# Kernel optimization log

Measured on AMD Instinct MI355X. Metric: run time of the kernel, lower is better.

## Reference

```python
import jax, jax.numpy as jnp
import numpy as np

NUM_ATOMS = 40000
NUM_EDGES = 640000
FAN_IN = 128
NFM = 128
FAN_OUT = 128


def setup_inputs() -> dict:
    key = jax.random.key(0)
    k1, k2, k3, k4, k5, k6, k7 = jax.random.split(key, 7)
    x = jax.random.normal(k1, (NUM_ATOMS, FAN_IN), dtype=jnp.float32)
    w_ij = jax.random.normal(k2, (NUM_EDGES, NFM), dtype=jnp.float32)
    seg_i = jnp.sort(jax.random.randint(k3, (NUM_EDGES,), 0, NUM_ATOMS))
    idx_j = jax.random.randint(k4, (NUM_EDGES,), 0, NUM_ATOMS)
    # learned params: in2fac (no bias), fac2out (bias)
    W_in = jax.random.normal(k5, (FAN_IN, NFM), dtype=jnp.float32) / np.sqrt(FAN_IN)
    W_out = jax.random.normal(k6, (NFM, FAN_OUT), dtype=jnp.float32) / np.sqrt(NFM)
    b_out = jax.random.normal(k7, (FAN_OUT,), dtype=jnp.float32) * 0.01
    return {"x": x, "w_ij": w_ij, "seg_i": seg_i, "idx_j": idx_j,
            "seg_i_sum": NUM_ATOMS, "W_in": W_in, "W_out": W_out, "b_out": b_out}


def reference(x, w_ij, seg_i, idx_j, seg_i_sum, W_in, W_out, b_out):
    # in2fac: Dense without bias  (num_atoms, nFM)
    f = x @ W_in
    # gather features of atom j per interaction  (num_edges, nFM)
    f_j = jnp.take(f, idx_j, axis=0)
    # elementwise filter multiply
    wf = w_ij * f_j
    # segment-sum pool over interactions of each atom i  (num_atoms, nFM)
    conv = jax.ops.segment_sum(wf, seg_i, num_segments=seg_i_sum)
    # fac2out: Dense with bias, activation=None
    return conv @ W_out + b_out
```

## Files before the change

kernel.cpp:

```cpp
#include <hip/hip_runtime.h>

#define NUM_ATOMS 40000
#define NUM_EDGES 640000

__global__ void k_rowstart(const int* __restrict__ seg, int* __restrict__ rs) {
  const int i = blockIdx.x * blockDim.x + threadIdx.x;
  if (i > NUM_ATOMS) return;
  int lo = 0, hi = NUM_EDGES;
  while (lo < hi) {
    const int mid = (lo + hi) >> 1;
    if (seg[mid] < i) lo = mid + 1; else hi = mid;
  }
  rs[i] = lo;
}

__global__ __launch_bounds__(512, 2) void k_gemm1(
    const float* __restrict__ x, const float* __restrict__ Win,
    float* __restrict__ f) {
  __shared__ float xT[128 * 128];
  __shared__ float Wl[128 * 128];
  const int t = threadIdx.x;
  const int m0 = blockIdx.x * 128;

  {
    const float4* Wg = (const float4*)Win;
    float4* Ws = (float4*)Wl;
#pragma unroll
    for (int i = 0; i < 8; ++i) Ws[t + i * 512] = Wg[t + i * 512];
  }
  {
    const int m = t & 127;
    const int kq = t >> 7;
    int mg = m0 + m;
    if (mg >= NUM_ATOMS) mg = NUM_ATOMS - 1;
    const float4* xg = (const float4*)(x + (size_t)mg * 128);
#pragma unroll
    for (int i = 0; i < 8; ++i) {
      const int k4 = kq + i * 4;
      const float4 v = xg[k4];
      const int k = k4 * 4;
      xT[(k + 0) * 128 + m] = v.x;
      xT[(k + 1) * 128 + m] = v.y;
      xT[(k + 2) * 128 + m] = v.z;
      xT[(k + 3) * 128 + m] = v.w;
    }
  }
  __syncthreads();

  const int tx = t & 31;
  const int ty = t >> 5;
  float acc[8][4];
#pragma unroll
  for (int i = 0; i < 8; ++i)
#pragma unroll
    for (int j = 0; j < 4; ++j) acc[i][j] = 0.f;

#pragma unroll 4
  for (int k = 0; k < 128; ++k) {
    const float4 a0 = *(const float4*)&xT[k * 128 + 4 * ty];
    const float4 a1 = *(const float4*)&xT[k * 128 + 64 + 4 * ty];
    const float2 b0 = *(const float2*)&Wl[k * 128 + 2 * tx];
    const float2 b1 = *(const float2*)&Wl[k * 128 + 64 + 2 * tx];
    const float av[8] = {a0.x, a0.y, a0.z, a0.w, a1.x, a1.y, a1.z, a1.w};
    const float bv[4] = {b0.x, b0.y, b1.x, b1.y};
#pragma unroll
    for (int i = 0; i < 8; ++i)
#pragma unroll
      for (int j = 0; j < 4; ++j) acc[i][j] += av[i] * bv[j];
  }

#pragma unroll
  for (int i = 0; i < 8; ++i) {
    const int m = (i < 4) ? (4 * ty + i) : (64 + 4 * ty + (i - 4));
    const int mg = m0 + m;
    if (mg < NUM_ATOMS) {
      float2* o = (float2*)(f + (size_t)mg * 128);
      o[tx]      = make_float2(acc[i][0], acc[i][1]);
      o[32 + tx] = make_float2(acc[i][2], acc[i][3]);
    }
  }
}

__global__ __launch_bounds__(256, 2) void k_conv_out(
    const float* __restrict__ f, const float* __restrict__ w_ij,
    const int* __restrict__ idx_j, const int* __restrict__ rs,
    const float* __restrict__ Wout, const float* __restrict__ bout,
    float* __restrict__ out) {
  __shared__ float Wl[128 * 128];
  __shared__ float conv[32 * 128];
  const int t = threadIdx.x;

  {
    const float4* Wg = (const float4*)Wout;
    float4* Ws = (float4*)Wl;
#pragma unroll
    for (int i = 0; i < 16; ++i) Ws[t + i * 256] = Wg[t + i * 256];
  }

  const int wv = t >> 6;
  const int l = t & 63;
  const int abase = blockIdx.x * 32;

#pragma unroll 1
  for (int ai = 0; ai < 8; ++ai) {
    const int al = wv * 8 + ai;
    const int a = abase + al;
    float accx = 0.f, accy = 0.f;
    const int e0 = rs[a];
    const int e1 = rs[a + 1];
    int e = e0;
    for (; e + 4 <= e1; e += 4) {
      const int j0 = idx_j[e + 0];
      const int j1 = idx_j[e + 1];
      const int j2 = idx_j[e + 2];
      const int j3 = idx_j[e + 3];
      const float2 w0 = ((const float2*)(w_ij + (size_t)(e + 0) * 128))[l];
      const float2 w1 = ((const float2*)(w_ij + (size_t)(e + 1) * 128))[l];
      const float2 w2 = ((const float2*)(w_ij + (size_t)(e + 2) * 128))[l];
      const float2 w3 = ((const float2*)(w_ij + (size_t)(e + 3) * 128))[l];
      const float2 f0 = ((const float2*)(f + (size_t)j0 * 128))[l];
      const float2 f1 = ((const float2*)(f + (size_t)j1 * 128))[l];
      const float2 f2 = ((const float2*)(f + (size_t)j2 * 128))[l];
      const float2 f3 = ((const float2*)(f + (size_t)j3 * 128))[l];
      accx += w0.x * f0.x; accy += w0.y * f0.y;
      accx += w1.x * f1.x; accy += w1.y * f1.y;
      accx += w2.x * f2.x; accy += w2.y * f2.y;
      accx += w3.x * f3.x; accy += w3.y * f3.y;
    }
    for (; e < e1; ++e) {
      const int j = idx_j[e];
      const float2 w = ((const float2*)(w_ij + (size_t)e * 128))[l];
      const float2 fv = ((const float2*)(f + (size_t)j * 128))[l];
      accx += w.x * fv.x; accy += w.y * fv.y;
    }
    ((float2*)(conv + al * 128))[l] = make_float2(accx, accy);
  }
  __syncthreads();

  const int tx = t & 31;
  const int ty = t >> 5;
  const float2 bb0 = ((const float2*)bout)[tx];
  const float2 bb1 = ((const float2*)bout)[32 + tx];
  float acc2[4][4];
#pragma unroll
  for (int i = 0; i < 4; ++i) {
    acc2[i][0] = bb0.x; acc2[i][1] = bb0.y;
    acc2[i][2] = bb1.x; acc2[i][3] = bb1.y;
  }
#pragma unroll 4
  for (int c = 0; c < 128; ++c) {
    const float2 b0 = *(const float2*)&Wl[c * 128 + 2 * tx];
    const float2 b1 = *(const float2*)&Wl[c * 128 + 64 + 2 * tx];
#pragma unroll
    for (int i = 0; i < 4; ++i) {
      const float cv = conv[(4 * ty + i) * 128 + c];
      acc2[i][0] += cv * b0.x;
      acc2[i][1] += cv * b0.y;
      acc2[i][2] += cv * b1.x;
      acc2[i][3] += cv * b1.y;
    }
  }
#pragma unroll
  for (int i = 0; i < 4; ++i) {
    const int a = abase + 4 * ty + i;
    float2* o = (float2*)(out + (size_t)a * 128);
    o[tx]      = make_float2(acc2[i][0], acc2[i][1]);
    o[32 + tx] = make_float2(acc2[i][2], acc2[i][3]);
  }
}

extern "C" void kernel_launch(void* const* d_in, const int* in_sizes, int n_in,
                              void* d_out, int out_size, void* d_ws, size_t ws_size,
                              hipStream_t stream) {
  const float* x    = (const float*)d_in[0];
  const float* w_ij = (const float*)d_in[1];
  const int*   seg  = (const int*)d_in[2];
  const int*   idxj = (const int*)d_in[3];
  const float* Win  = (const float*)d_in[5];
  const float* Wout = (const float*)d_in[6];
  const float* bout = (const float*)d_in[7];
  float* out = (float*)d_out;

  float* f = (float*)d_ws;
  int* rs = (int*)((char*)d_ws + (size_t)NUM_ATOMS * 128 * sizeof(float));

  k_rowstart<<<(NUM_ATOMS + 1 + 255) / 256, 256, 0, stream>>>(seg, rs);
  k_gemm1<<<(NUM_ATOMS + 127) / 128, 512, 0, stream>>>(x, Win, f);
  k_conv_out<<<NUM_ATOMS / 32, 256, 0, stream>>>(f, w_ij, idxj, rs, Wout, bout, out);
}
```

Before: 584.7 us.

## Unfuse output GEMM from conv and coalesce idx_j loads via wave shuffles

```diff
diff --git a/kernel.cpp b/kernel.cpp
--- a/kernel.cpp
+++ b/kernel.cpp
@@ -14,16 +14,16 @@
   rs[i] = lo;
 }
 
-__global__ __launch_bounds__(512, 2) void k_gemm1(
-    const float* __restrict__ x, const float* __restrict__ Win,
-    float* __restrict__ f) {
-  __shared__ float xT[128 * 128];
+__global__ __launch_bounds__(512, 2) void k_gemm128(
+    const float* __restrict__ A, const float* __restrict__ W,
+    const float* __restrict__ bias, float* __restrict__ out) {
+  __shared__ float AT[128 * 128];
   __shared__ float Wl[128 * 128];
   const int t = threadIdx.x;
   const int m0 = blockIdx.x * 128;
 
   {
-    const float4* Wg = (const float4*)Win;
+    const float4* Wg = (const float4*)W;
     float4* Ws = (float4*)Wl;
 #pragma unroll
     for (int i = 0; i < 8; ++i) Ws[t + i * 512] = Wg[t + i * 512];
@@ -33,32 +33,39 @@
     const int kq = t >> 7;
     int mg = m0 + m;
     if (mg >= NUM_ATOMS) mg = NUM_ATOMS - 1;
-    const float4* xg = (const float4*)(x + (size_t)mg * 128);
+    const float4* ag = (const float4*)(A + (size_t)mg * 128);
 #pragma unroll
     for (int i = 0; i < 8; ++i) {
       const int k4 = kq + i * 4;
-      const float4 v = xg[k4];
+      const float4 v = ag[k4];
       const int k = k4 * 4;
-      xT[(k + 0) * 128 + m] = v.x;
-      xT[(k + 1) * 128 + m] = v.y;
-      xT[(k + 2) * 128 + m] = v.z;
-      xT[(k + 3) * 128 + m] = v.w;
+      AT[(k + 0) * 128 + m] = v.x;
+      AT[(k + 1) * 128 + m] = v.y;
+      AT[(k + 2) * 128 + m] = v.z;
+      AT[(k + 3) * 128 + m] = v.w;
     }
   }
   __syncthreads();
 
   const int tx = t & 31;
   const int ty = t >> 5;
+
+  float binit[4] = {0.f, 0.f, 0.f, 0.f};
+  if (bias != nullptr) {
+    const float2 bb0 = ((const float2*)bias)[tx];
+    const float2 bb1 = ((const float2*)bias)[32 + tx];
+    binit[0] = bb0.x; binit[1] = bb0.y; binit[2] = bb1.x; binit[3] = bb1.y;
+  }
   float acc[8][4];
 #pragma unroll
   for (int i = 0; i < 8; ++i)
 #pragma unroll
-    for (int j = 0; j < 4; ++j) acc[i][j] = 0.f;
+    for (int j = 0; j < 4; ++j) acc[i][j] = binit[j];
 
 #pragma unroll 4
   for (int k = 0; k < 128; ++k) {
-    const float4 a0 = *(const float4*)&xT[k * 128 + 4 * ty];
-    const float4 a1 = *(const float4*)&xT[k * 128 + 64 + 4 * ty];
+    const float4 a0 = *(const float4*)&AT[k * 128 + 4 * ty];
+    const float4 a1 = *(const float4*)&AT[k * 128 + 64 + 4 * ty];
     const float2 b0 = *(const float2*)&Wl[k * 128 + 2 * tx];
     const float2 b1 = *(const float2*)&Wl[k * 128 + 64 + 2 * tx];
     const float av[8] = {a0.x, a0.y, a0.z, a0.w, a1.x, a1.y, a1.z, a1.w};
@@ -74,50 +81,39 @@
     const int m = (i < 4) ? (4 * ty + i) : (64 + 4 * ty + (i - 4));
     const int mg = m0 + m;
     if (mg < NUM_ATOMS) {
-      float2* o = (float2*)(f + (size_t)mg * 128);
+      float2* o = (float2*)(out + (size_t)mg * 128);
       o[tx]      = make_float2(acc[i][0], acc[i][1]);
       o[32 + tx] = make_float2(acc[i][2], acc[i][3]);
     }
   }
 }
 
-__global__ __launch_bounds__(256, 2) void k_conv_out(
+__global__ __launch_bounds__(256) void k_conv(
     const float* __restrict__ f, const float* __restrict__ w_ij,
     const int* __restrict__ idx_j, const int* __restrict__ rs,
-    const float* __restrict__ Wout, const float* __restrict__ bout,
-    float* __restrict__ out) {
-  __shared__ float Wl[128 * 128];
-  __shared__ float conv[32 * 128];
-  const int t = threadIdx.x;
+    float* __restrict__ conv) {
+  const int wv = threadIdx.x >> 6;
+  const int l = threadIdx.x & 63;
+  const int a = blockIdx.x * 4 + wv;
 
-  {
-    const float4* Wg = (const float4*)Wout;
-    float4* Ws = (float4*)Wl;
-#pragma unroll
-    for (int i = 0; i < 16; ++i) Ws[t + i * 256] = Wg[t + i * 256];
-  }
+  const int e0 = rs[a];
+  const int e1 = rs[a + 1];
+  float accx = 0.f, accy = 0.f;
 
-  const int wv = t >> 6;
-  const int l = t & 63;
-  const int abase = blockIdx.x * 32;
-
-#pragma unroll 1
-  for (int ai = 0; ai < 8; ++ai) {
-    const int al = wv * 8 + ai;
-    const int a = abase + al;
-    float accx = 0.f, accy = 0.f;
-    const int e0 = rs[a];
-    const int e1 = rs[a + 1];
-    int e = e0;
-    for (; e + 4 <= e1; e += 4) {
-      const int j0 = idx_j[e + 0];
-      const int j1 = idx_j[e + 1];
-      const int j2 = idx_j[e + 2];
-      const int j3 = idx_j[e + 3];
-      const float2 w0 = ((const float2*)(w_ij + (size_t)(e + 0) * 128))[l];
-      const float2 w1 = ((const float2*)(w_ij + (size_t)(e + 1) * 128))[l];
-      const float2 w2 = ((const float2*)(w_ij + (size_t)(e + 2) * 128))[l];
-      const float2 w3 = ((const float2*)(w_ij + (size_t)(e + 3) * 128))[l];
+  for (int base = e0; base < e1; base += 64) {
+    const int n = min(64, e1 - base);
+    int j = 0;
+    if (l < n) j = idx_j[base + l];
+    int k = 0;
+    for (; k + 4 <= n; k += 4) {
+      const int j0 = __shfl(j, k + 0);
+      const int j1 = __shfl(j, k + 1);
+      const int j2 = __shfl(j, k + 2);
+      const int j3 = __shfl(j, k + 3);
+      const float2 w0 = ((const float2*)(w_ij + (size_t)(base + k + 0) * 128))[l];
+      const float2 w1 = ((const float2*)(w_ij + (size_t)(base + k + 1) * 128))[l];
+      const float2 w2 = ((const float2*)(w_ij + (size_t)(base + k + 2) * 128))[l];
+      const float2 w3 = ((const float2*)(w_ij + (size_t)(base + k + 3) * 128))[l];
       const float2 f0 = ((const float2*)(f + (size_t)j0 * 128))[l];
       const float2 f1 = ((const float2*)(f + (size_t)j1 * 128))[l];
       const float2 f2 = ((const float2*)(f + (size_t)j2 * 128))[l];
@@ -127,46 +123,14 @@
       accx += w2.x * f2.x; accy += w2.y * f2.y;
       accx += w3.x * f3.x; accy += w3.y * f3.y;
     }
-    for (; e < e1; ++e) {
-      const int j = idx_j[e];
-      const float2 w = ((const float2*)(w_ij + (size_t)e * 128))[l];
-      const float2 fv = ((const float2*)(f + (size_t)j * 128))[l];
+    for (; k < n; ++k) {
+      const int jk = __shfl(j, k);
+      const float2 w = ((const float2*)(w_ij + (size_t)(base + k) * 128))[l];
+      const float2 fv = ((const float2*)(f + (size_t)jk * 128))[l];
       accx += w.x * fv.x; accy += w.y * fv.y;
     }
-    ((float2*)(conv + al * 128))[l] = make_float2(accx, accy);
   }
-  __syncthreads();
-
-  const int tx = t & 31;
-  const int ty = t >> 5;
-  const float2 bb0 = ((const float2*)bout)[tx];
-  const float2 bb1 = ((const float2*)bout)[32 + tx];
-  float acc2[4][4];
-#pragma unroll
-  for (int i = 0; i < 4; ++i) {
-    acc2[i][0] = bb0.x; acc2[i][1] = bb0.y;
-    acc2[i][2] = bb1.x; acc2[i][3] = bb1.y;
-  }
-#pragma unroll 4
-  for (int c = 0; c < 128; ++c) {
-    const float2 b0 = *(const float2*)&Wl[c * 128 + 2 * tx];
-    const float2 b1 = *(const float2*)&Wl[c * 128 + 64 + 2 * tx];
-#pragma unroll
-    for (int i = 0; i < 4; ++i) {
-      const float cv = conv[(4 * ty + i) * 128 + c];
-      acc2[i][0] += cv * b0.x;
-      acc2[i][1] += cv * b0.y;
-      acc2[i][2] += cv * b1.x;
-      acc2[i][3] += cv * b1.y;
-    }
-  }
-#pragma unroll
-  for (int i = 0; i < 4; ++i) {
-    const int a = abase + 4 * ty + i;
-    float2* o = (float2*)(out + (size_t)a * 128);
-    o[tx]      = make_float2(acc2[i][0], acc2[i][1]);
-    o[32 + tx] = make_float2(acc2[i][2], acc2[i][3]);
-  }
+  ((float2*)(conv + (size_t)a * 128))[l] = make_float2(accx, accy);
 }
 
 extern "C" void kernel_launch(void* const* d_in, const int* in_sizes, int n_in,
@@ -181,10 +145,12 @@
   const float* bout = (const float*)d_in[7];
   float* out = (float*)d_out;
 
-  float* f = (float*)d_ws;
-  int* rs = (int*)((char*)d_ws + (size_t)NUM_ATOMS * 128 * sizeof(float));
+  float* f    = (float*)d_ws;
+  float* conv = (float*)((char*)d_ws + (size_t)NUM_ATOMS * 128 * sizeof(float));
+  int*   rs   = (int*)((char*)d_ws + 2 * (size_t)NUM_ATOMS * 128 * sizeof(float));
 
   k_rowstart<<<(NUM_ATOMS + 1 + 255) / 256, 256, 0, stream>>>(seg, rs);
-  k_gemm1<<<(NUM_ATOMS + 127) / 128, 512, 0, stream>>>(x, Win, f);
-  k_conv_out<<<NUM_ATOMS / 32, 256, 0, stream>>>(f, w_ij, idxj, rs, Wout, bout, out);
+  k_gemm128<<<(NUM_ATOMS + 127) / 128, 512, 0, stream>>>(x, Win, nullptr, f);
+  k_conv<<<NUM_ATOMS / 4, 256, 0, stream>>>(f, w_ij, idxj, rs, conv);
+  k_gemm128<<<(NUM_ATOMS + 127) / 128, 512, 0, stream>>>(conv, Wout, bout, out);
 }
```

New measurement: 547.5 us. -6.4%, faster.
